# Kernel tuning notes

Measured on AMD Instinct MI355X. Metric: run time of the kernel, lower is better.

## Reference

```python
import jax, jax.numpy as jnp
import numpy as np

GAMMA = 0.99
EPS = 1e-05
K = 8192   # num_embeddings
D = 256    # embed_dim
B, T = 32, 1024

def setup_inputs() -> dict:
    key = jax.random.key(0)
    k1, k2 = jax.random.split(key)
    ze = jax.random.normal(k1, (B, T, D), dtype=jnp.float32)
    embedW = jax.random.normal(k2, (K, D), dtype=jnp.float32)
    mt = jnp.zeros((K, D), dtype=jnp.float32)
    Nt = jnp.zeros((K,), dtype=jnp.float32)
    return {"ze": ze, "embedW": embedW, "mt": mt, "Nt": Nt}

def reference(ze, embedW, mt, Nt):
    b = ze.shape[0]
    ze_flat = ze.reshape(-1, ze.shape[-1])                      # [N, D]
    # squared euclidean distances: ||z||^2 - 2 z W^T + ||w||^2  -> [N, K]
    dist_mat = (jnp.sum(ze_flat * ze_flat, axis=1, keepdims=True)
                - 2.0 * ze_flat @ embedW.T
                + jnp.sum(embedW * embedW, axis=1)[None, :])
    zq_idx = jnp.argmin(dist_mat, axis=-1)                      # [N]
    zq = embedW[zq_idx]                                         # gather [N, D]
    # EMA codebook update (training mode), one-hot scatter expressed as segment sums
    nt = jax.ops.segment_sum(jnp.ones_like(zq_idx, dtype=jnp.float32), zq_idx, num_segments=K)
    Nt_new = GAMMA * Nt + (1.0 - GAMMA) * nt
    st = jax.ops.segment_sum(ze_flat, zq_idx, num_segments=K)   # one_hot.T @ ze
    mt_new = GAMMA * mt + (1.0 - GAMMA) * st
    n = jnp.sum(Nt_new)
    Nn = (Nt_new + EPS) * n / (n + K * EPS)
    embedW_new = mt_new / Nn[:, None]
    zq = zq.reshape(b, -1, zq.shape[-1])                        # [B, T, D]
    zq_idx = zq_idx.reshape(b, -1)                              # [B, T]
    commit = jnp.mean((jax.lax.stop_gradient(zq) - ze) ** 2)
    zq_st = ze + jax.lax.stop_gradient(zq - ze)                 # straight-through
    return (zq_st, commit, zq_idx, embedW_new, mt_new, Nt_new)
```

## Files before the change

kernel.cpp:

```cpp
#include <hip/hip_runtime.h>
#include <cstddef>
#include <cstdint>

#define GAMMA_F 0.99f
#define OMG_F   0.01f
#define EPS_F   1e-5f
#define KN 8192
#define DD 256
#define NN 32768

#define OFF_ZQ     0
#define OFF_COMMIT 8388608
#define OFF_IDX    8388609
#define OFF_EMB    8421377
#define OFF_MT     10518529
#define OFF_NT     12615681

#define C1 32
#define NCH1 (NN / C1)
#define NREC (NCH1 * 2)
#define C2 32
#define NCH2 (NREC / C2)

typedef _Float16 half8 __attribute__((ext_vector_type(8)));
typedef _Float16 half4 __attribute__((ext_vector_type(4)));
typedef float    f32x4 __attribute__((ext_vector_type(4)));
typedef unsigned long long u64;

__device__ __forceinline__ void gload16(const void* g, void* l) {
    __builtin_amdgcn_global_load_lds(
        (const __attribute__((address_space(1))) unsigned int*)g,
        (__attribute__((address_space(3))) unsigned int*)l, 16, 0, 0);
}

__device__ __forceinline__ u64 packdi(float dist, int n) {
    unsigned u = __float_as_uint(dist);
    u ^= (unsigned)((int)u >> 31) | 0x80000000u;
    return ((u64)u << 32) | (unsigned)n;
}

__global__ __launch_bounds__(256) void prep_kernel(
    const float* __restrict__ ze, const float* __restrict__ W,
    _Float16* __restrict__ zh, _Float16* __restrict__ wh,
    float* __restrict__ wsq, unsigned* __restrict__ hist_zero) {
    const int tid = threadIdx.x;
    const size_t gid = (size_t)blockIdx.x * 256 + tid;

    {
        const size_t i0 = gid * 4;
        const float4 v = *(const float4*)(ze + i0);
        half4 h;
        h[0] = (_Float16)v.x; h[1] = (_Float16)v.y;
        h[2] = (_Float16)v.z; h[3] = (_Float16)v.w;
        *(half4*)(zh + i0) = h;
    }
    if (gid < KN) hist_zero[gid] = 0u;

    if (blockIdx.x < KN / 4) {
        const int k = blockIdx.x * 4 + (tid >> 6);
        const int lane = tid & 63;
        const float4 v = *(const float4*)(W + (size_t)k * DD + lane * 4);
        half4 h;
        h[0] = (_Float16)v.x; h[1] = (_Float16)v.y;
        h[2] = (_Float16)v.z; h[3] = (_Float16)v.w;
        *(half4*)(wh + (size_t)k * DD + lane * 4) = h;
        float s = v.x * v.x + v.y * v.y + v.z * v.z + v.w * v.w;
#pragma unroll
        for (int off = 32; off > 0; off >>= 1) s += __shfl_down(s, off, 64);
        if (lane == 0) wsq[k] = s;
    }
}

__global__ __launch_bounds__(256, 4) void screen_kernel(
    const _Float16* __restrict__ zh, const _Float16* __restrict__ wh,
    const float* __restrict__ wsq,
    unsigned* __restrict__ tlo, unsigned* __restrict__ thi) {
    __shared__ __align__(16) _Float16 As[128 * 64];
    __shared__ __align__(16) _Float16 Bs[128 * 64];
    __shared__ __align__(16) u64 top2[128][2];

    const int tid  = threadIdx.x;
    const int wave = tid >> 6;
    const int lane = tid & 63;
    const int quad = lane >> 4;
    const int col  = lane & 15;
    const int ph = wave & 1;
    const int ch = wave >> 1;
    const int pw = ph * 64;
    const int cw = ch * 64;

    const int bm = blockIdx.x >> 6;
    const int bn = blockIdx.x & 63;
    const int m0 = bm * 128;
    const int n0 = bn * 128;

    f32x4 acc[4][4];
#pragma unroll
    for (int i = 0; i < 4; i++)
#pragma unroll
        for (int j = 0; j < 4; j++) acc[i][j] = (f32x4){0.f, 0.f, 0.f, 0.f};

    for (int c = 0; c < 4; ++c) {
        const int d0 = c * 64;
        __syncthreads();
#pragma unroll
        for (int i = 0; i < 4; ++i) {
            const int clin = (wave * 4 + i) * 64 + lane;
            const int mrow = clin >> 3;
            const int p = clin & 7;
            const int q = p ^ (mrow & 7);
            gload16(zh + (size_t)(m0 + mrow) * DD + d0 + q * 8,
                    As + (wave * 4 + i) * 512);
            gload16(wh + (size_t)(n0 + mrow) * DD + d0 + q * 8,
                    Bs + (wave * 4 + i) * 512);
        }
        __syncthreads();

#pragma unroll
        for (int kk = 0; kk < 2; ++kk) {
            half8 a[4], b[4];
#pragma unroll
            for (int t = 0; t < 4; ++t) {
                const int cr = cw + t * 16 + col;
                const int pr = pw + t * 16 + col;
                const int cc = kk * 4 + quad;
                a[t] = *(const half8*)(Bs + cr * 64 + (cc ^ (cr & 7)) * 8);
                b[t] = *(const half8*)(As + pr * 64 + (cc ^ (pr & 7)) * 8);
            }
#pragma unroll
            for (int ci = 0; ci < 4; ++ci)
#pragma unroll
                for (int pj = 0; pj < 4; ++pj)
                    acc[ci][pj] = __builtin_amdgcn_mfma_f32_16x16x32_f16(
                        a[ci], b[pj], acc[ci][pj], 0, 0, 0);
        }
    }

    float wq[4][4];
#pragma unroll
    for (int ci = 0; ci < 4; ++ci) {
        const float4 t = *(const float4*)(wsq + n0 + cw + ci * 16 + quad * 4);
        wq[ci][0] = t.x + 4096.f; wq[ci][1] = t.y + 4096.f;
        wq[ci][2] = t.z + 4096.f; wq[ci][3] = t.w + 4096.f;
    }
    const unsigned base7 = (unsigned)(cw + quad * 4);

#pragma unroll
    for (int pj = 0; pj < 4; ++pj) {
        unsigned t0 = 0xFFFFFFFFu, t1 = 0xFFFFFFFFu;
#pragma unroll
        for (int ci = 0; ci < 4; ++ci)
#pragma unroll
            for (int v = 0; v < 4; ++v) {
                const float dist = fmaf(-2.0f, acc[ci][pj][v], wq[ci][v]);
                const unsigned x = (__float_as_uint(dist) & ~127u) |
                                   (base7 + ci * 16 + v);
                const unsigned mx = t0 > x ? t0 : x;
                t0 = t0 < x ? t0 : x;
                t1 = t1 < mx ? t1 : mx;
            }
#pragma unroll
        for (int mk = 16; mk < 64; mk <<= 1) {
            const unsigned o0 = __shfl_xor(t0, mk, 64);
            const unsigned o1 = __shfl_xor(t1, mk, 64);
            const unsigned lo = t0 < o0 ? t0 : o0;
            const unsigned hi = t0 < o0 ? o0 : t0;
            const unsigned mn = t1 < o1 ? t1 : o1;
            t0 = lo;
            t1 = hi < mn ? hi : mn;
        }
        if (quad == 0)
            top2[pw + pj * 16 + col][ch] = ((u64)t1 << 32) | t0;
    }
    __syncthreads();
    if (tid < 128) {
        const u64 e0 = top2[tid][0], e1 = top2[tid][1];
        const unsigned a0 = (unsigned)e0, a1 = (unsigned)(e0 >> 32);
        const unsigned b0 = (unsigned)e1, b1 = (unsigned)(e1 >> 32);
        const unsigned t0 = a0 < b0 ? a0 : b0;
        const unsigned hi = a0 < b0 ? b0 : a0;
        const unsigned mn = a1 < b1 ? a1 : b1;
        const unsigned t1 = hi < mn ? hi : mn;
        const unsigned c1 = n0 + (t0 & 127u);
        const unsigned c2 = n0 + (t1 & 127u);
        const u64 ent = (u64)(t0 & ~127u) | ((u64)c1 << 32) | ((u64)c2 << 48);
        tlo[(size_t)bn * NN + m0 + tid] = (unsigned)ent;
        thi[(size_t)bn * NN + m0 + tid] = (unsigned)(ent >> 32);
    }
}

__global__ __launch_bounds__(256) void select_kernel(
    const unsigned* __restrict__ tlo, const unsigned* __restrict__ thi,
    const float* __restrict__ ze, const float* __restrict__ W,
    float* __restrict__ idxf, float* __restrict__ zq_out,
    unsigned* __restrict__ hist, float* __restrict__ partials) {
    __shared__ unsigned sl[4][32];
    __shared__ float wsum[4];
    const int tid = threadIdx.x;
    const int lane = tid & 63;
    const int w = tid >> 6;

    const int n = blockIdx.x * 4 + w;
    const unsigned elo = tlo[(size_t)lane * NN + n];
    const unsigned ehi = thi[(size_t)lane * NN + n];
    const float d1 = __uint_as_float(elo);
    float mn = d1;
#pragma unroll
    for (int off = 32; off > 0; off >>= 1)
        mn = fminf(mn, __shfl_xor(mn, off, 64));
    const bool q = d1 <= mn + 1.0f;
    const u64 bal = __ballot(q);
    if (q) {
        const int rank = __popcll(bal & ((1ull << lane) - 1ull));
        if (rank < 16) {
            sl[w][2 * rank + 0] = ehi & 0xffffu;
            sl[w][2 * rank + 1] = ehi >> 16;
        }
    }
    unsigned m = 2u * (unsigned)__popcll(bal);
    m = m < 32u ? m : 32u;
    __syncthreads();

    const float4 z = *(const float4*)(ze + (size_t)n * DD + lane * 4);
    u64 best = ~0ull;
    for (unsigned j = 0; j < m; ++j) {
        const unsigned c = sl[w][j];
        const float4 ww = *(const float4*)(W + (size_t)c * DD + lane * 4);
        float dot = z.x * ww.x + z.y * ww.y + z.z * ww.z + z.w * ww.w;
        float wq  = ww.x * ww.x + ww.y * ww.y + ww.z * ww.z + ww.w * ww.w;
#pragma unroll
        for (int off = 32; off > 0; off >>= 1) {
            dot += __shfl_xor(dot, off, 64);
            wq  += __shfl_xor(wq, off, 64);
        }
        const float dist = fmaf(-2.0f, dot, wq);
        const u64 pk = packdi(dist, (int)c);
        best = best < pk ? best : pk;
    }
    const int idx = (int)(unsigned)(best & 0xFFFFFFFFull);
    if (lane == 0) {
        idxf[n] = (float)idx;
        atomicAdd(hist + idx, 1u);
    }

    const float4 ww = *(const float4*)(W + (size_t)idx * DD + lane * 4);
    float4 d, o;
    d.x = ww.x - z.x; d.y = ww.y - z.y; d.z = ww.z - z.z; d.w = ww.w - z.w;
    o.x = z.x + d.x; o.y = z.y + d.y; o.z = z.z + d.z; o.w = z.w + d.w;
    *(float4*)(zq_out + (size_t)n * DD + lane * 4) = o;

    float c = d.x * d.x + d.y * d.y + d.z * d.z + d.w * d.w;
#pragma unroll
    for (int off = 32; off > 0; off >>= 1) c += __shfl_down(c, off, 64);

    if (lane == 0) wsum[w] = c;
    __syncthreads();
    if (tid == 0)
        partials[4 * blockIdx.x] = wsum[0] + wsum[1] + wsum[2] + wsum[3];
}

__global__ __launch_bounds__(256) void prefix_kernel(
    const float* __restrict__ Nt_in, float* __restrict__ ntn,
    const float* __restrict__ partials, float* __restrict__ commit_out,
    unsigned* __restrict__ offsets, float* __restrict__ nws) {
    const int t = threadIdx.x;
    unsigned* hist = (unsigned*)ntn;
    const int base = t * 32;
    unsigned loc[32];
    unsigned sum = 0;
#pragma unroll
    for (int i = 0; i < 32; ++i) { loc[i] = hist[base + i]; sum += loc[i]; }

    __shared__ unsigned ssum[256];
    __shared__ float cred[256];
    __shared__ float fred[256];
    ssum[t] = sum;
    float cp = 0.f;
    for (int i = t; i < NN / 4; i += 256) cp += partials[4 * i];
    cred[t] = cp;
    __syncthreads();

    for (int off = 1; off < 256; off <<= 1) {
        const unsigned v = (t >= off) ? ssum[t - off] : 0u;
        __syncthreads();
        ssum[t] += v;
        __syncthreads();
    }
    unsigned run = (t > 0) ? ssum[t - 1] : 0u;

    for (int off = 128; off > 0; off >>= 1) {
        if (t < off) cred[t] += cred[t + off];
        __syncthreads();
    }
    if (t == 0) *commit_out = cred[0] * (1.0f / 8388608.0f);

#pragma unroll
    for (int i = 0; i < 32; ++i) {
        offsets[base + i] = run;
        run += loc[i];
    }
    float fs = 0.f;
#pragma unroll
    for (int i = 0; i < 32; ++i) {
        const float v = GAMMA_F * Nt_in[base + i] + OMG_F * (float)loc[i];
        ntn[base + i] = v;
        fs += v;
    }
    fred[t] = fs;
    __syncthreads();
    for (int off = 128; off > 0; off >>= 1) {
        if (t < off) fred[t] += fred[t + off];
        __syncthreads();
    }
    if (t == 0) nws[0] = fred[0];
}

__global__ __launch_bounds__(256) void scatter_kernel(
    const float* __restrict__ idxf, unsigned* __restrict__ offsets,
    unsigned* __restrict__ perm, unsigned* __restrict__ codes,
    const float* __restrict__ mt_in, float* __restrict__ mt_out) {
    const size_t gid = (size_t)blockIdx.x * 256 + threadIdx.x;
    {
        const float4 m = *(const float4*)(mt_in + gid * 4);
        float4 r;
        r.x = GAMMA_F * m.x; r.y = GAMMA_F * m.y;
        r.z = GAMMA_F * m.z; r.w = GAMMA_F * m.w;
        *(float4*)(mt_out + gid * 4) = r;
    }
    if (gid < NN) {
        const int idx = (int)idxf[gid];
        const unsigned pos = atomicAdd(offsets + idx, 1u);
        perm[pos] = (unsigned)gid;
        codes[pos] = (unsigned)idx;
    }
}

__global__ __launch_bounds__(256) void mt1_kernel(
    const float* __restrict__ ze, const float* __restrict__ mt_in,
    const unsigned* __restrict__ perm, const unsigned* __restrict__ codes,
    float* __restrict__ mt_out, unsigned* __restrict__ prec,
    float* __restrict__ pdata) {
    const int tid = threadIdx.x;
    const int lane = tid & 63;
    const int w = blockIdx.x * 4 + (tid >> 6);
    const int j0 = w * C1;

    unsigned ccur = codes[j0];
    bool first = true;
    float4 acc = {0.f, 0.f, 0.f, 0.f};

    for (int j = j0; j < j0 + C1; ++j) {
        const unsigned c = codes[j];
        if (c != ccur) {
            if (first) {
                *(float4*)(pdata + (size_t)(2 * w) * DD + lane * 4) = acc;
                if (lane == 0) prec[2 * w] = ccur;
                first = false;
            } else {
                const size_t o = (size_t)ccur * DD + lane * 4;
                const float4 m = *(const float4*)(mt_in + o);
                float4 r;
                r.x = GAMMA_F * m.x + OMG_F * acc.x;
                r.y = GAMMA_F * m.y + OMG_F * acc.y;
                r.z = GAMMA_F * m.z + OMG_F * acc.z;
                r.w = GAMMA_F * m.w + OMG_F * acc.w;
                *(float4*)(mt_out + o) = r;
            }
            acc = (float4){0.f, 0.f, 0.f, 0.f};
            ccur = c;
        }
        const unsigned p = perm[j];
        const float4 z = *(const float4*)(ze + (size_t)p * DD + lane * 4);
        acc.x += z.x; acc.y += z.y; acc.z += z.z; acc.w += z.w;
    }
    if (first) {
        *(float4*)(pdata + (size_t)(2 * w) * DD + lane * 4) = acc;
        *(float4*)(pdata + (size_t)(2 * w + 1) * DD + lane * 4) =
            (float4){0.f, 0.f, 0.f, 0.f};
        if (lane == 0) { prec[2 * w] = ccur; prec[2 * w + 1] = ccur; }
    } else {
        *(float4*)(pdata + (size_t)(2 * w + 1) * DD + lane * 4) = acc;
        if (lane == 0) prec[2 * w + 1] = ccur;
    }
}

__global__ __launch_bounds__(256) void mt2_kernel(
    const float* __restrict__ mt_in, const unsigned* __restrict__ prec,
    const float* __restrict__ pdata, float* __restrict__ mt_out) {
    const int tid = threadIdx.x;
    const int lane = tid & 63;
    const int w = blockIdx.x * 4 + (tid >> 6);
    const int r0 = w * C2;

    unsigned ccur = prec[r0];
    bool first = true;
    float4 acc = {0.f, 0.f, 0.f, 0.f};

    for (int r = r0; r < r0 + C2; ++r) {
        const unsigned c = prec[r];
        if (c != ccur) {
            if (first) {
                float* mp = mt_out + (size_t)ccur * DD + lane * 4;
                atomicAdd(mp + 0, OMG_F * acc.x);
                atomicAdd(mp + 1, OMG_F * acc.y);
                atomicAdd(mp + 2, OMG_F * acc.z);
                atomicAdd(mp + 3, OMG_F * acc.w);
                first = false;
            } else {
                const size_t o = (size_t)ccur * DD + lane * 4;
                const float4 m = *(const float4*)(mt_in + o);
                float4 rr;
                rr.x = GAMMA_F * m.x + OMG_F * acc.x;
                rr.y = GAMMA_F * m.y + OMG_F * acc.y;
                rr.z = GAMMA_F * m.z + OMG_F * acc.z;
                rr.w = GAMMA_F * m.w + OMG_F * acc.w;
                *(float4*)(mt_out + o) = rr;
            }
            acc = (float4){0.f, 0.f, 0.f, 0.f};
            ccur = c;
        }
        const float4 v = *(const float4*)(pdata + (size_t)r * DD + lane * 4);
        acc.x += v.x; acc.y += v.y; acc.z += v.z; acc.w += v.w;
    }
    float* mp = mt_out + (size_t)ccur * DD + lane * 4;
    atomicAdd(mp + 0, OMG_F * acc.x);
    atomicAdd(mp + 1, OMG_F * acc.y);
    atomicAdd(mp + 2, OMG_F * acc.z);
    atomicAdd(mp + 3, OMG_F * acc.w);
}

__global__ __launch_bounds__(256) void final_kernel(
    const float* __restrict__ nt_new, const float* __restrict__ mt_new,
    const float* __restrict__ nws, float* __restrict__ emb_out) {
    const float n = nws[0];
    const size_t i0 = ((size_t)blockIdx.x * 256 + threadIdx.x) * 4;
    const int k = (int)(i0 >> 8);

    const float4 mt = *(const float4*)(mt_new + i0);
    const float Nn = (nt_new[k] + EPS_F) * n / (n + (float)KN * EPS_F);
    float4 e;
    e.x = mt.x / Nn;
    e.y = mt.y / Nn;
    e.z = mt.z / Nn;
    e.w = mt.w / Nn;
    *(float4*)(emb_out + i0) = e;
}

extern "C" void kernel_launch(void* const* d_in, const int* in_sizes, int n_in,
                              void* d_out, int out_size, void* d_ws, size_t ws_size,
                              hipStream_t stream) {
    const float* ze = (const float*)d_in[0];
    const float* W  = (const float*)d_in[1];
    const float* mt = (const float*)d_in[2];
    const float* Nt = (const float*)d_in[3];

    float* out    = (float*)d_out;
    float* zq_out = out + OFF_ZQ;
    float* commit = out + OFF_COMMIT;
    float* idxf   = out + OFF_IDX;
    float* emb    = out + OFF_EMB;
    float* mtn    = out + OFF_MT;
    float* ntn    = out + OFF_NT;

    _Float16* zh = (_Float16*)zq_out;
    _Float16* wh = (_Float16*)(zq_out + (size_t)NN * DD / 2);
    float* wsqbuf = zq_out + (size_t)NN * DD / 2 + (size_t)KN * DD / 2;
    unsigned* tlo = (unsigned*)emb;
    unsigned* thi = tlo + (size_t)64 * NN;
    float* partials = (float*)tlo;
    unsigned* offsets = tlo;
    unsigned* perm    = tlo + 8192;
    unsigned* codes   = tlo + 40960;
    unsigned* prec    = tlo + 73728;
    float*    pdata   = (float*)tlo + 75779;
    unsigned* hist    = (unsigned*)ntn;
    float*    nws     = (float*)d_ws;

    prep_kernel<<<(NN * DD / 4) / 256, 256, 0, stream>>>(
        ze, W, zh, wh, wsqbuf, hist);

    screen_kernel<<<(NN / 128) * (KN / 128), 256, 0, stream>>>(
        zh, wh, wsqbuf, tlo, thi);

    select_kernel<<<NN / 4, 256, 0, stream>>>(
        tlo, thi, ze, W, idxf, zq_out, hist, partials);

    prefix_kernel<<<1, 256, 0, stream>>>(Nt, ntn, partials, commit,
                                         offsets, nws);

    scatter_kernel<<<(KN * DD / 4) / 256, 256, 0, stream>>>(
        idxf, offsets, perm, codes, mt, mtn);

    mt1_kernel<<<NCH1 / 4, 256, 0, stream>>>(ze, mt, perm, codes, mtn,
                                             prec, pdata);

    mt2_kernel<<<NCH2 / 4, 256, 0, stream>>>(mt, prec, pdata, mtn);

    final_kernel<<<(KN * DD / 4) / 256, 256, 0, stream>>>(ntn, mtn, nws, emb);
}
```

Before: 362.7 us.

## Aggregate histogram and scatter atomics in shared memory, unroll candidate loop by two

Removes the per-row global atomic histogram from select_kernel and adds a separate hist_kernel that bins indices in a shared-memory histogram before flushing nonzero counts to global memory. The scatter kernel likewise reserves offsets per block through shared-memory counts, so it issues one global atomic per code per block instead of one per row. The candidate rescoring loop in select_kernel is unrolled by two so the two W loads and shuffle reductions can overlap. This costs an extra kernel launch and 32KB of LDS per block. Order within a code segment becomes block-grouped but stays a valid permutation.

After: 371.8 us. 1.03x slower.

```diff
diff --git a/kernel.cpp b/kernel.cpp
--- a/kernel.cpp
+++ b/kernel.cpp
@@ -193,7 +193,7 @@
     const unsigned* __restrict__ tlo, const unsigned* __restrict__ thi,
     const float* __restrict__ ze, const float* __restrict__ W,
     float* __restrict__ idxf, float* __restrict__ zq_out,
-    unsigned* __restrict__ hist, float* __restrict__ partials) {
+    float* __restrict__ partials) {
     __shared__ unsigned sl[4][32];
     __shared__ float wsum[4];
     const int tid = threadIdx.x;
@@ -223,25 +223,43 @@
 
     const float4 z = *(const float4*)(ze + (size_t)n * DD + lane * 4);
     u64 best = ~0ull;
-    for (unsigned j = 0; j < m; ++j) {
-        const unsigned c = sl[w][j];
-        const float4 ww = *(const float4*)(W + (size_t)c * DD + lane * 4);
-        float dot = z.x * ww.x + z.y * ww.y + z.z * ww.z + z.w * ww.w;
-        float wq  = ww.x * ww.x + ww.y * ww.y + ww.z * ww.z + ww.w * ww.w;
+    unsigned j = 0;
+    for (; j + 2 <= m; j += 2) {
+        const unsigned c0 = sl[w][j];
+        const unsigned c1 = sl[w][j + 1];
+        const float4 w0 = *(const float4*)(W + (size_t)c0 * DD + lane * 4);
+        const float4 w1 = *(const float4*)(W + (size_t)c1 * DD + lane * 4);
+        float d0 = z.x * w0.x + z.y * w0.y + z.z * w0.z + z.w * w0.w;
+        float q0 = w0.x * w0.x + w0.y * w0.y + w0.z * w0.z + w0.w * w0.w;
+        float d1c = z.x * w1.x + z.y * w1.y + z.z * w1.z + z.w * w1.w;
+        float q1 = w1.x * w1.x + w1.y * w1.y + w1.z * w1.z + w1.w * w1.w;
 #pragma unroll
         for (int off = 32; off > 0; off >>= 1) {
-            dot += __shfl_xor(dot, off, 64);
-            wq  += __shfl_xor(wq, off, 64);
-        }
-        const float dist = fmaf(-2.0f, dot, wq);
-        const u64 pk = packdi(dist, (int)c);
-        best = best < pk ? best : pk;
+            d0  += __shfl_xor(d0, off, 64);
+            q0  += __shfl_xor(q0, off, 64);
+            d1c += __shfl_xor(d1c, off, 64);
+            q1  += __shfl_xor(q1, off, 64);
+        }
+        const u64 p0 = packdi(fmaf(-2.0f, d0, q0), (int)c0);
+        const u64 p1 = packdi(fmaf(-2.0f, d1c, q1), (int)c1);
+        const u64 pm = p0 < p1 ? p0 : p1;
+        best = best < pm ? best : pm;
+    }
+    if (j < m) {
+        const unsigned c0 = sl[w][j];
+        const float4 w0 = *(const float4*)(W + (size_t)c0 * DD + lane * 4);
+        float d0 = z.x * w0.x + z.y * w0.y + z.z * w0.z + z.w * w0.w;
+        float q0 = w0.x * w0.x + w0.y * w0.y + w0.z * w0.z + w0.w * w0.w;
+#pragma unroll
+        for (int off = 32; off > 0; off >>= 1) {
+            d0 += __shfl_xor(d0, off, 64);
+            q0 += __shfl_xor(q0, off, 64);
+        }
+        const u64 p0 = packdi(fmaf(-2.0f, d0, q0), (int)c0);
+        best = best < p0 ? best : p0;
     }
     const int idx = (int)(unsigned)(best & 0xFFFFFFFFull);
-    if (lane == 0) {
-        idxf[n] = (float)idx;
-        atomicAdd(hist + idx, 1u);
-    }
+    if (lane == 0) idxf[n] = (float)idx;
 
     const float4 ww = *(const float4*)(W + (size_t)idx * DD + lane * 4);
     float4 d, o;
@@ -257,6 +275,22 @@
     __syncthreads();
     if (tid == 0)
         partials[4 * blockIdx.x] = wsum[0] + wsum[1] + wsum[2] + wsum[3];
+}
+
+__global__ __launch_bounds__(256) void hist_kernel(
+    const float* __restrict__ idxf, unsigned* __restrict__ hist) {
+    __shared__ unsigned h[KN];
+    const int t = threadIdx.x;
+    for (int i = t; i < KN; i += 256) h[i] = 0u;
+    __syncthreads();
+    const int n = blockIdx.x * 256 + t;
+    const int idx = (int)idxf[n];
+    atomicAdd(&h[idx], 1u);
+    __syncthreads();
+    for (int i = t; i < KN; i += 256) {
+        const unsigned c = h[i];
+        if (c) atomicAdd(hist + i, c);
+    }
 }
 
 __global__ __launch_bounds__(256) void prefix_kernel(
@@ -319,7 +353,9 @@
     const float* __restrict__ idxf, unsigned* __restrict__ offsets,
     unsigned* __restrict__ perm, unsigned* __restrict__ codes,
     const float* __restrict__ mt_in, float* __restrict__ mt_out) {
-    const size_t gid = (size_t)blockIdx.x * 256 + threadIdx.x;
+    __shared__ unsigned h[KN];
+    const int t = threadIdx.x;
+    const size_t gid = (size_t)blockIdx.x * 256 + t;
     {
         const float4 m = *(const float4*)(mt_in + gid * 4);
         float4 r;
@@ -327,9 +363,18 @@
         r.z = GAMMA_F * m.z; r.w = GAMMA_F * m.w;
         *(float4*)(mt_out + gid * 4) = r;
     }
-    if (gid < NN) {
+    if (blockIdx.x < NN / 256) {
+        for (int i = t; i < KN; i += 256) h[i] = 0u;
+        __syncthreads();
         const int idx = (int)idxf[gid];
-        const unsigned pos = atomicAdd(offsets + idx, 1u);
+        const unsigned r = atomicAdd(&h[idx], 1u);
+        __syncthreads();
+        for (int i = t; i < KN; i += 256) {
+            const unsigned c = h[i];
+            if (c) h[i] = atomicAdd(offsets + i, c);
+        }
+        __syncthreads();
+        const unsigned pos = h[idx] + r;
         perm[pos] = (unsigned)gid;
         codes[pos] = (unsigned)idx;
     }
@@ -483,7 +528,9 @@
         zh, wh, wsqbuf, tlo, thi);
 
     select_kernel<<<NN / 4, 256, 0, stream>>>(
-        tlo, thi, ze, W, idxf, zq_out, hist, partials);
+        tlo, thi, ze, W, idxf, zq_out, partials);
+
+    hist_kernel<<<NN / 256, 256, 0, stream>>>(idxf, hist);
 
     prefix_kernel<<<1, 256, 0, stream>>>(Nt, ntn, partials, commit,
                                          offsets, nws);
```
